# Kernel optimization log

Measured on AMD Instinct MI355X. Metric: run time of the kernel, lower is better.

## Reference

```python
import jax, jax.numpy as jnp
import numpy as np

H, W = 256, 256
N = 1024          # gaussians
G = 2             # num_gabor
RANK = 6          # abundance channels / endmembers
C = 128           # spectral bands
LORA_ALPHA = 0.1


def setup_inputs() -> dict:
    key = jax.random.key(0)
    ks = jax.random.split(key, 8)
    xyz = 0.5 * jax.random.normal(ks[0], (N, 2), jnp.float32)          # pre-tanh means
    cholesky = jnp.zeros((N, 3), jnp.float32)                           # + bound -> identity-ish cov
    feat0 = jnp.log(jnp.expm1(jnp.float32(0.05)))                       # inverse softplus(0.05)
    features_dc = feat0 + 0.01 * jax.random.normal(ks[1], (N, RANK), jnp.float32)
    gabor_freqs = (jax.random.uniform(ks[2], (N * G, 2), jnp.float32) - 0.5) * 0.002
    gabor_weights = jax.random.uniform(ks[3], (N * G, 1), jnp.float32) * -5.0
    lora_U = 0.3 * jax.random.normal(ks[4], (RANK, 2), jnp.float32)
    lora_V = 0.001 * jax.random.normal(ks[5], (2, C), jnp.float32)
    lora_scale_logit = jnp.zeros((1,), jnp.float32)
    opacity = jnp.ones((N, 1), jnp.float32)
    endmember = jax.random.uniform(ks[6], (RANK, C), jnp.float32)
    return {"xyz": xyz, "cholesky": cholesky, "features_dc": features_dc,
            "gabor_freqs": gabor_freqs, "gabor_weights": gabor_weights,
            "lora_U": lora_U, "lora_V": lora_V, "lora_scale_logit": lora_scale_logit,
            "opacity": opacity, "endmember": endmember}


def _rasterize_gabor_sum(xyz, cholesky, features_dc, gabor_freqs, gabor_weights, opacity):
    # project_gaussians_2d: tanh means in [-1,1] -> pixel coords
    means = jnp.tanh(xyz)                                               # [N,2]
    centers = (means * 0.5 + 0.5) * jnp.array([W, H], jnp.float32)      # [N,2] (x,y)
    ch = cholesky + jnp.array([0.5, 0.0, 0.5], jnp.float32)             # cholesky bound
    l1, l2, l3 = ch[:, 0], ch[:, 1], ch[:, 2]
    # Sigma = L L^T, L = [[l1,0],[l2,l3]] -> conic = Sigma^{-1}
    a = l1 * l1
    b = l1 * l2
    c = l2 * l2 + l3 * l3
    det = a * c - b * b
    ca, cb, cc = c / det, -b / det, a / det                             # [N]
    # pixel grid, row-major flat index p = y*W + x, pixel centers at +0.5
    xs = jnp.arange(W, dtype=jnp.float32) + 0.5
    ys = jnp.arange(H, dtype=jnp.float32) + 0.5
    px = jnp.tile(xs, H)                                                # [HW]
    py = jnp.repeat(ys, W)                                              # [HW]
    dx = px[None, :] - centers[:, 0:1]                                  # [N,HW]
    dy = py[None, :] - centers[:, 1:2]                                  # [N,HW]
    sigma = 0.5 * (ca[:, None] * dx * dx + cc[:, None] * dy * dy) + cb[:, None] * dx * dy
    gauss = jnp.where(sigma >= 0, jnp.exp(-sigma), 0.0)                 # [N,HW]
    # gabor modulation: 1 + sum_g w_g * cos(fx_g*dx + fy_g*dy)
    fx = jnp.exp(gabor_freqs[:, 0]).reshape(N, G)
    fy = jnp.exp(gabor_freqs[:, 1]).reshape(N, G)
    gw = jax.nn.sigmoid(gabor_weights[:, 0]).reshape(N, G)
    mod = jnp.ones_like(gauss)
    for g in range(G):  # small fixed loop over gabor components
        mod = mod + gw[:, g:g + 1] * jnp.cos(fx[:, g:g + 1] * dx + fy[:, g:g + 1] * dy)
    wmat = gauss * mod                                                  # [N,HW]
    feats = jax.nn.softplus(features_dc) * opacity                      # [N,RANK]
    # sum-blending rasterization (background = 0); linear in features so
    # the 3/4-channel group split in the original concatenates to the same result
    abundance = jnp.einsum('np,nr->pr', wmat, feats)                    # [HW,RANK]
    return jnp.maximum(abundance, 0.0)


def reference(xyz, cholesky, features_dc, gabor_freqs, gabor_weights,
              lora_U, lora_V, lora_scale_logit, opacity, endmember):
    abundance = _rasterize_gabor_sum(xyz, cholesky, features_dc,
                                     gabor_freqs, gabor_weights, opacity)
    # LoRA-calibrated endmember
    delta = jnp.tanh(lora_U @ lora_V)                                   # [RANK,C]
    scale = LORA_ALPHA * jnp.tanh(lora_scale_logit[0])
    E = jnp.clip(endmember + scale * delta, 1e-6, None)
    render = (abundance @ E).reshape(1, H, W, C).transpose(0, 3, 1, 2)  # [1,C,H,W]
    return render, abundance, E
```

## Files before the change

### kernel.cpp

```cpp
#include <hip/hip_runtime.h>
#include <math.h>

#define HH 256
#define WW 256
#define NPTS 1024
#define RANK 6
#define NC 128
#define PIX (HH * WW)
#define CGRP 4
#define CHB (NC / CGRP)
#define PSTRIDE 20
#define MAXG 256
#define SEG 128
#define TPAD 264

typedef float vf4 __attribute__((ext_vector_type(4)));

__device__ __forceinline__ float softplus_f(float x) {
    return fmaxf(x, 0.0f) + log1pf(__expf(-fabsf(x)));
}

__global__ __launch_bounds__(256) void fused_kernel(
    const float* __restrict__ xyz, const float* __restrict__ chol,
    const float* __restrict__ fdc, const float* __restrict__ gfreq,
    const float* __restrict__ gwt, const float* __restrict__ opac,
    const float* __restrict__ lU, const float* __restrict__ lV,
    const float* __restrict__ lS, const float* __restrict__ em,
    float* __restrict__ render, float* __restrict__ abund,
    float* __restrict__ Eout)
{
    __shared__ float Els[CHB * 8];
    __shared__ float glist[MAXG * PSTRIDE];
    __shared__ int   idxl[4 * SEG];
    __shared__ int   wcnt[4];
    __shared__ float accT[RANK * TPAD];

    const int t    = threadIdx.x;
    const int bid  = blockIdx.x;
    const int cg   = bid & 3;
    const int tile = bid >> 2;
    const int tx   = (tile & 3) * 64;
    const int ty   = (tile >> 2) * 4;
    const float px = (float)(tx + (t & 63)) + 0.5f;
    const float py = (float)(ty + (t >> 6)) + 0.5f;
    const int wv   = t >> 6;
    const int ln   = t & 63;

    {
        float scale = 0.1f * tanhf(lS[0]);
        if (t < CHB * RANK) {
            int r = t >> 5; int cl = t & 31; int c = cg * CHB + cl;
            float dot = lU[r * 2] * lV[c] + lU[r * 2 + 1] * lV[NC + c];
            Els[cl * 8 + r] = fmaxf(em[r * NC + c] + scale * tanhf(dot), 1e-6f);
        }
        if (bid == 0) {
            for (int i = t; i < RANK * NC; i += 256) {
                int r = i >> 7; int c = i & 127;
                float dot = lU[r * 2] * lV[c] + lU[r * 2 + 1] * lV[NC + c];
                Eout[i] = fmaxf(em[i] + scale * tanhf(dot), 1e-6f);
            }
        }
    }

    const float txmin = (float)tx, txmax = (float)(tx + 64);
    const float tymin = (float)ty, tymax = (float)(ty + 4);
    {
        int cnt = 0;
        const int gbase = wv * 256;
        for (int k = 0; k < 4; ++k) {
            const int gid = gbase + k * 64 + ln;
            float cx = (tanhf(xyz[gid * 2 + 0]) * 0.5f + 0.5f) * (float)WW;
            float cy = (tanhf(xyz[gid * 2 + 1]) * 0.5f + 0.5f) * (float)HH;
            float l1 = chol[gid * 3 + 0] + 0.5f;
            float l2 = chol[gid * 3 + 1];
            float l3 = chol[gid * 3 + 2] + 0.5f;
            float a = l1 * l1;
            float c = l2 * l2 + l3 * l3;
            float rx = 6.0f * sqrtf(a);
            float ry = 6.0f * sqrtf(c);
            bool hit = (cx - rx <= txmax) && (cx + rx >= txmin) &&
                       (cy - ry <= tymax) && (cy + ry >= tymin);
            unsigned long long m = __ballot(hit);
            if (hit) {
                int pos = cnt + __popcll(m & ((1ull << ln) - 1ull));
                if (pos < SEG) idxl[wv * SEG + pos] = gid;
            }
            cnt += __popcll(m);
        }
        if (ln == 0) wcnt[wv] = min(cnt, SEG);
    }
    __syncthreads();

    const int c0 = wcnt[0], c1 = wcnt[1], c2 = wcnt[2], c3 = wcnt[3];
    const int o1 = c0, o2 = c0 + c1, o3 = o2 + c2;
    int T = o3 + c3;
    if (T > MAXG) T = MAXG;

    for (int j = t; j < T; j += 256) {
        int w, o;
        if (j < o1)      { w = 0; o = j; }
        else if (j < o2) { w = 1; o = j - o1; }
        else if (j < o3) { w = 2; o = j - o2; }
        else             { w = 3; o = j - o3; }
        const int n = idxl[w * SEG + o];
        float cx = (tanhf(xyz[n * 2 + 0]) * 0.5f + 0.5f) * (float)WW;
        float cy = (tanhf(xyz[n * 2 + 1]) * 0.5f + 0.5f) * (float)HH;
        float l1 = chol[n * 3 + 0] + 0.5f;
        float l2 = chol[n * 3 + 1];
        float l3 = chol[n * 3 + 2] + 0.5f;
        float a = l1 * l1, bb = l1 * l2, c = l2 * l2 + l3 * l3;
        float inv = 1.0f / (a * c - bb * bb);
        float* g = glist + j * PSTRIDE;
        g[0] = cx; g[1] = cy;
        g[2] = c * inv; g[3] = -bb * inv; g[4] = a * inv;
        g[5] = __expf(gfreq[n * 4 + 0]);
        g[6] = __expf(gfreq[n * 4 + 1]);
        g[7] = __expf(gfreq[n * 4 + 2]);
        g[8] = __expf(gfreq[n * 4 + 3]);
        g[9]  = 1.0f / (1.0f + __expf(-gwt[n * 2 + 0]));
        g[10] = 1.0f / (1.0f + __expf(-gwt[n * 2 + 1]));
        float op = opac[n];
#pragma unroll
        for (int r = 0; r < RANK; ++r)
            g[11 + r] = softplus_f(fdc[n * RANK + r]) * op;
    }
    __syncthreads();

    float acc[RANK] = {0.f, 0.f, 0.f, 0.f, 0.f, 0.f};
    for (int i = 0; i < T; ++i) {
        const vf4* gv = (const vf4*)(glist + i * PSTRIDE);
        vf4 g0 = gv[0];
        vf4 g1 = gv[1];
        vf4 g2 = gv[2];
        float dx = px - g0.x;
        float dy = py - g0.y;
        float sigma = 0.5f * (g0.z * dx * dx + g1.x * dy * dy) + g0.w * dx * dy;
        vf4 g3 = gv[3];
        vf4 g4 = gv[4];
        float wm = __expf(-sigma) *
                   (1.0f + g2.y * __cosf(g1.y * dx + g1.z * dy)
                         + g2.z * __cosf(g1.w * dx + g2.x * dy));
        wm = (sigma >= 0.0f) ? wm : 0.0f;
        acc[0] = fmaf(wm, g2.w, acc[0]);
        acc[1] = fmaf(wm, g3.x, acc[1]);
        acc[2] = fmaf(wm, g3.y, acc[2]);
        acc[3] = fmaf(wm, g3.z, acc[3]);
        acc[4] = fmaf(wm, g3.w, acc[4]);
        acc[5] = fmaf(wm, g4.x, acc[5]);
    }
#pragma unroll
    for (int r = 0; r < RANK; ++r) acc[r] = fmaxf(acc[r], 0.0f);

#pragma unroll
    for (int r = 0; r < RANK; ++r)
        accT[r * TPAD + t] = acc[r];
    __syncthreads();

    const int u   = t & 63;
    const int wv2 = t >> 6;
    const int row = u >> 4;
    const int xg  = u & 15;
    const int p0  = (ty + row) * WW + tx + xg * 4;

    vf4 ab[RANK];
#pragma unroll
    for (int r = 0; r < RANK; ++r)
        ab[r] = *(const vf4*)(accT + r * TPAD + 4 * u);

    if (cg == 0 && wv2 == 0) {
        vf4* ao = (vf4*)(abund + (size_t)p0 * RANK);
        vf4 q0 = { ab[0][0], ab[1][0], ab[2][0], ab[3][0] };
        vf4 q1 = { ab[4][0], ab[5][0], ab[0][1], ab[1][1] };
        vf4 q2 = { ab[2][1], ab[3][1], ab[4][1], ab[5][1] };
        vf4 q3 = { ab[0][2], ab[1][2], ab[2][2], ab[3][2] };
        vf4 q4 = { ab[4][2], ab[5][2], ab[0][3], ab[1][3] };
        vf4 q5 = { ab[2][3], ab[3][3], ab[4][3], ab[5][3] };
        __builtin_nontemporal_store(q0, ao + 0);
        __builtin_nontemporal_store(q1, ao + 1);
        __builtin_nontemporal_store(q2, ao + 2);
        __builtin_nontemporal_store(q3, ao + 3);
        __builtin_nontemporal_store(q4, ao + 4);
        __builtin_nontemporal_store(q5, ao + 5);
    }

    float* rp = render + (size_t)cg * CHB * PIX + p0;
#pragma unroll
    for (int i = 0; i < CHB / 4; ++i) {
        const int cl = wv2 * (CHB / 4) + i;
        const vf4 e0 = *(const vf4*)(Els + cl * 8);
        const vf4 e1 = *(const vf4*)(Els + cl * 8 + 4);
        vf4 o = ab[0] * e0.x;
        o += ab[1] * e0.y;
        o += ab[2] * e0.z;
        o += ab[3] * e0.w;
        o += ab[4] * e1.x;
        o += ab[5] * e1.y;
        __builtin_nontemporal_store(o, (vf4*)(rp + (size_t)cl * PIX));
    }
}

extern "C" void kernel_launch(void* const* d_in, const int* in_sizes, int n_in,
                              void* d_out, int out_size, void* d_ws, size_t ws_size,
                              hipStream_t stream)
{
    const float* xyz             = (const float*)d_in[0];
    const float* cholesky        = (const float*)d_in[1];
    const float* features_dc     = (const float*)d_in[2];
    const float* gabor_freqs     = (const float*)d_in[3];
    const float* gabor_weights   = (const float*)d_in[4];
    const float* lora_U          = (const float*)d_in[5];
    const float* lora_V          = (const float*)d_in[6];
    const float* lora_scale_logit= (const float*)d_in[7];
    const float* opacity         = (const float*)d_in[8];
    const float* endmember       = (const float*)d_in[9];

    float* out    = (float*)d_out;
    float* render = out;
    float* abund  = out + (size_t)NC * PIX;
    float* Eout   = abund + (size_t)PIX * RANK;

    fused_kernel<<<1024, 256, 0, stream>>>(
        xyz, cholesky, features_dc, gabor_freqs, gabor_weights, opacity,
        lora_U, lora_V, lora_scale_logit, endmember, render, abund, Eout);
}
```

Baseline: 21.74 us.

## Split gaussian loop across waves per row tile instead of replicating per channel group

```diff
diff --git a/kernel.cpp b/kernel.cpp
--- a/kernel.cpp
+++ b/kernel.cpp
@@ -7,12 +7,9 @@
 #define RANK 6
 #define NC 128
 #define PIX (HH * WW)
-#define CGRP 4
-#define CHB (NC / CGRP)
 #define PSTRIDE 20
-#define MAXG 256
+#define MAXG 160
 #define SEG 128
-#define TPAD 264
 
 typedef float vf4 __attribute__((ext_vector_type(4)));
 
@@ -29,41 +26,37 @@
     float* __restrict__ render, float* __restrict__ abund,
     float* __restrict__ Eout)
 {
-    __shared__ float Els[CHB * 8];
+    __shared__ float Els[NC * 8];
     __shared__ float glist[MAXG * PSTRIDE];
     __shared__ int   idxl[4 * SEG];
     __shared__ int   wcnt[4];
-    __shared__ float accT[RANK * TPAD];
+    __shared__ float accT[RANK * 4 * 64];
+    __shared__ float accR[RANK * 64];
 
     const int t    = threadIdx.x;
-    const int bid  = blockIdx.x;
-    const int cg   = bid & 3;
-    const int tile = bid >> 2;
+    const int tile = blockIdx.x;
     const int tx   = (tile & 3) * 64;
-    const int ty   = (tile >> 2) * 4;
-    const float px = (float)(tx + (t & 63)) + 0.5f;
-    const float py = (float)(ty + (t >> 6)) + 0.5f;
+    const int ty   = tile >> 2;
     const int wv   = t >> 6;
     const int ln   = t & 63;
+    const float px = (float)(tx + ln) + 0.5f;
+    const float py = (float)ty + 0.5f;
 
     {
         float scale = 0.1f * tanhf(lS[0]);
-        if (t < CHB * RANK) {
-            int r = t >> 5; int cl = t & 31; int c = cg * CHB + cl;
+#pragma unroll
+        for (int k = 0; k < 3; ++k) {
+            int i = k * 256 + t;
+            int r = i >> 7; int c = i & 127;
             float dot = lU[r * 2] * lV[c] + lU[r * 2 + 1] * lV[NC + c];
-            Els[cl * 8 + r] = fmaxf(em[r * NC + c] + scale * tanhf(dot), 1e-6f);
+            float e = fmaxf(em[i] + scale * tanhf(dot), 1e-6f);
+            Els[c * 8 + r] = e;
+            if (tile == 0) Eout[i] = e;
         }
-        if (bid == 0) {
-            for (int i = t; i < RANK * NC; i += 256) {
-                int r = i >> 7; int c = i & 127;
-                float dot = lU[r * 2] * lV[c] + lU[r * 2 + 1] * lV[NC + c];
-                Eout[i] = fmaxf(em[i] + scale * tanhf(dot), 1e-6f);
-            }
-        }
     }
 
     const float txmin = (float)tx, txmax = (float)(tx + 64);
-    const float tymin = (float)ty, tymax = (float)(ty + 4);
+    const float tymin = (float)ty, tymax = (float)(ty + 1);
     {
         int cnt = 0;
         const int gbase = wv * 256;
@@ -127,7 +120,7 @@
     __syncthreads();
 
     float acc[RANK] = {0.f, 0.f, 0.f, 0.f, 0.f, 0.f};
-    for (int i = 0; i < T; ++i) {
+    for (int i = wv; i < T; i += 4) {
         const vf4* gv = (const vf4*)(glist + i * PSTRIDE);
         vf4 g0 = gv[0];
         vf4 g1 = gv[1];
@@ -149,44 +142,41 @@
         acc[5] = fmaf(wm, g4.x, acc[5]);
     }
 #pragma unroll
-    for (int r = 0; r < RANK; ++r) acc[r] = fmaxf(acc[r], 0.0f);
-
-#pragma unroll
     for (int r = 0; r < RANK; ++r)
-        accT[r * TPAD + t] = acc[r];
-    __syncthreads();
-
-    const int u   = t & 63;
-    const int wv2 = t >> 6;
-    const int row = u >> 4;
-    const int xg  = u & 15;
-    const int p0  = (ty + row) * WW + tx + xg * 4;
-
+        accT[r * 256 + t] = acc[r];
+    __syncthreads();
+
+    for (int v = t; v < RANK * 64; v += 256) {
+        int r = v >> 6, u = v & 63;
+        const float* row = accT + r * 256;
+        float s = (row[u] + row[64 + u]) + (row[128 + u] + row[192 + u]);
+        accR[v] = fmaxf(s, 0.0f);
+    }
+    __syncthreads();
+
+    if (t < 96) {
+        vf4 q;
+#pragma unroll
+        for (int k = 0; k < 4; ++k) {
+            int v = t * 4 + k;
+            int pl = v / 6;
+            int r  = v - pl * 6;
+            q[k] = accR[r * 64 + pl];
+        }
+        __builtin_nontemporal_store(
+            q, (vf4*)(abund + (size_t)(ty * WW + tx) * RANK) + t);
+    }
+
+    const int pxo = (ln & 15) * 4;
     vf4 ab[RANK];
 #pragma unroll
     for (int r = 0; r < RANK; ++r)
-        ab[r] = *(const vf4*)(accT + r * TPAD + 4 * u);
-
-    if (cg == 0 && wv2 == 0) {
-        vf4* ao = (vf4*)(abund + (size_t)p0 * RANK);
-        vf4 q0 = { ab[0][0], ab[1][0], ab[2][0], ab[3][0] };
-        vf4 q1 = { ab[4][0], ab[5][0], ab[0][1], ab[1][1] };
-        vf4 q2 = { ab[2][1], ab[3][1], ab[4][1], ab[5][1] };
-        vf4 q3 = { ab[0][2], ab[1][2], ab[2][2], ab[3][2] };
-        vf4 q4 = { ab[4][2], ab[5][2], ab[0][3], ab[1][3] };
-        vf4 q5 = { ab[2][3], ab[3][3], ab[4][3], ab[5][3] };
-        __builtin_nontemporal_store(q0, ao + 0);
-        __builtin_nontemporal_store(q1, ao + 1);
-        __builtin_nontemporal_store(q2, ao + 2);
-        __builtin_nontemporal_store(q3, ao + 3);
-        __builtin_nontemporal_store(q4, ao + 4);
-        __builtin_nontemporal_store(q5, ao + 5);
-    }
-
-    float* rp = render + (size_t)cg * CHB * PIX + p0;
-#pragma unroll
-    for (int i = 0; i < CHB / 4; ++i) {
-        const int cl = wv2 * (CHB / 4) + i;
+        ab[r] = *(const vf4*)(accR + r * 64 + pxo);
+
+    float* rp = render + ty * WW + tx + pxo;
+#pragma unroll
+    for (int i = 0; i < 8; ++i) {
+        const int cl = wv * 32 + i * 4 + (ln >> 4);
         const vf4 e0 = *(const vf4*)(Els + cl * 8);
         const vf4 e1 = *(const vf4*)(Els + cl * 8 + 4);
         vf4 o = ab[0] * e0.x;
```

Result: faster. 17.69 us (-18.6%).
